# Optimization experiments

Hardware: AMD Instinct MI355X
Metric: run time of the kernel (lower is better)

## Reference

```python
import jax, jax.numpy as jnp
import numpy as np

HEADS = 8
DIM_HEAD = 64
SCALE = DIM_HEAD ** -0.5
POS_DIM = 64


def _sincos_pe(H, W, dim, dtype):
    # matches build_2d_sincos_pos_embed: [1, dim, H, W]
    y = jnp.linspace(-1.0, 1.0, H)[:, None] * jnp.ones((1, W), jnp.float32)
    x = jnp.ones((H, 1), jnp.float32) * jnp.linspace(-1.0, 1.0, W)[None, :]
    omega = 1.0 / (10000.0 ** (jnp.arange(dim // 4, dtype=jnp.float32) / (dim // 4)))
    px = x[..., None] * omega  # [H, W, dim//4]
    py = y[..., None] * omega
    pe = jnp.concatenate([jnp.sin(px), jnp.cos(px), jnp.sin(py), jnp.cos(py)], axis=-1)
    return pe.transpose(2, 0, 1)[None].astype(dtype)


def _conv2d(x, w):
    return jax.lax.conv_general_dilated(
        x, w, (1, 1), 'SAME', dimension_numbers=('NCHW', 'OIHW', 'NCHW'))


def _sobel(d):
    kx = jnp.array([[1, 0, -1], [2, 0, -2], [1, 0, -1]], jnp.float32).reshape(1, 1, 3, 3)
    ky = jnp.array([[1, 2, 1], [0, 0, 0], [-1, -2, -1]], jnp.float32).reshape(1, 1, 3, 3)
    return _conv2d(d, kx), _conv2d(d, ky)


def setup_inputs() -> dict:
    key = jax.random.key(0)
    ks = jax.random.split(key, 8)
    B, C, H, W = 2, 256, 64, 64
    hid = HEADS * DIM_HEAD  # 512
    s = 0.02
    return {
        'x': jax.random.normal(ks[0], (B, C, H, W), jnp.float32),
        'dsm': jax.random.uniform(ks[1], (B, 1, H, W), jnp.float32),
        'wq': jax.random.normal(ks[2], (hid, C), jnp.float32) * s,
        'wkv': jax.random.normal(ks[3], (2 * hid, C + 1), jnp.float32) * s,
        'wout': jax.random.normal(ks[4], (C, hid), jnp.float32) * s,
        'bout': jnp.zeros((C,), jnp.float32),
        'w_hape': jax.random.normal(ks[5], (hid, POS_DIM + 3), jnp.float32) * s,
        'b_hape': jnp.zeros((hid,), jnp.float32),
        'w_alpha': jax.random.normal(ks[6], (1, 1, 3, 3), jnp.float32) * 0.1,
        'b_alpha': jnp.zeros((1,), jnp.float32),
    }


def reference(x, dsm, wq, wkv, wout, bout, w_hape, b_hape, w_alpha, b_alpha):
    B, C, H, W = x.shape
    hid = wq.shape[0]
    # per-sample min-max normalize DSM over spatial dims
    dmin = dsm.min(axis=(2, 3), keepdims=True)
    dmax = dsm.max(axis=(2, 3), keepdims=True)
    d = (dsm - dmin) / (dmax - dmin + 1e-6)
    # HAPE: [PE | h | grad_h] -> 1x1 conv to hidden
    pe = jnp.broadcast_to(_sincos_pe(H, W, POS_DIM, x.dtype), (B, POS_DIM, H, W))
    gx, gy = _sobel(d)
    hape_in = jnp.concatenate([pe, d, gx, gy], axis=1)  # [B, 67, H, W]
    hape_k = jnp.einsum('oc,bchw->bohw', w_hape, hape_in) + b_hape[None, :, None, None]
    # QKV via 1x1 convs
    q = jnp.einsum('oc,bchw->bohw', wq, x)
    kv = jnp.einsum('oc,bchw->bohw', wkv, jnp.concatenate([x, d], axis=1))
    k = kv[:, :hid] + hape_k
    v = kv[:, hid:]
    to_heads = lambda t: t.reshape(B, HEADS, DIM_HEAD, H * W)  # b (h c) x y -> b h c (xy)
    qh = to_heads(q) * SCALE
    kh = to_heads(k)
    vh = to_heads(v)
    sim = jnp.einsum('bhdi,bhdj->bhij', qh, kh)  # [B, h, N, N]
    attn = jax.nn.softmax(sim, axis=-1)
    out = jnp.einsum('bhij,bhdj->bhid', attn, vh)  # [B, h, N, d]
    # b h (x y) d -> b (h d) x y
    out = out.transpose(0, 1, 3, 2).reshape(B, HEADS * DIM_HEAD, H, W)
    out = jnp.einsum('oc,bchw->bohw', wout, out) + bout[None, :, None, None]
    # fine: gradient-magnitude alpha gating
    mag = jnp.sqrt(jnp.maximum(gx, 0.0) ** 2 + jnp.maximum(gy, 0.0) ** 2 + 1e-12)
    alpha = jax.nn.sigmoid(_conv2d(mag, w_alpha) + b_alpha[None, :, None, None])
    return x + out * alpha
```

## Files before the change

kernel.cpp:

```cpp
#include <hip/hip_runtime.h>
#include <math.h>

#define NPOS 4096
#define MTOT 8192
#define KP   352
#define HT 64
#define WT 64
#define NSPLIT 2
#define KEYS_PER (NPOS / NSPLIT)
#define NCH (KEYS_PER / 64)

typedef unsigned short ushortT;
typedef short v8s __attribute__((ext_vector_type(8)));
typedef float v4f __attribute__((ext_vector_type(4)));
typedef unsigned uint2v __attribute__((ext_vector_type(2)));

static __device__ __forceinline__ ushortT bfr(float f) {
    union { float f; unsigned u; } v; v.f = f;
    return (ushortT)((v.u + 0x8000u) >> 16);
}
static __device__ __forceinline__ unsigned pack2bf(float a, float b) {
    union { float f; unsigned u; } ua, ub; ua.f = a; ub.f = b;
    return __builtin_amdgcn_perm(ub.u + 0x8000u, ua.u + 0x8000u, 0x07060302u);
}
static __device__ __forceinline__ unsigned pack2bf_t(float a, float b) {
    union { float f; unsigned u; } ua, ub; ua.f = a; ub.f = b;
    return __builtin_amdgcn_perm(ub.u, ua.u, 0x07060302u);
}
static __device__ __forceinline__ float fexp2(float x) {
#if __has_builtin(__builtin_amdgcn_exp2f)
    return __builtin_amdgcn_exp2f(x);
#else
    return exp2f(x);
#endif
}
static __device__ __forceinline__ void gll16(const ushortT* g, ushortT* l) {
    __builtin_amdgcn_global_load_lds((const __attribute__((address_space(1))) void*)g,
                                     (__attribute__((address_space(3))) void*)l, 16, 0, 0);
}

__global__ void k_prep(const float* __restrict__ dsm,
                       const float* __restrict__ walpha, const float* __restrict__ balpha,
                       ushortT* __restrict__ F, float* __restrict__ alpha) {
    int idx = blockIdx.x * 256 + threadIdx.x;
    int b = idx / NPOS, n = idx % NPOS;
    int hh = n / WT, ww = n % WT;
    const float* dp = dsm + (size_t)b * NPOS;

    float mn = 1e30f, mx = -1e30f;
    for (int i = threadIdx.x; i < NPOS; i += 256) {
        float v = dp[i];
        mn = fminf(mn, v); mx = fmaxf(mx, v);
    }
    for (int off = 32; off; off >>= 1) {
        mn = fminf(mn, __shfl_xor(mn, off, 64));
        mx = fmaxf(mx, __shfl_xor(mx, off, 64));
    }
    __shared__ float smn[4], smx[4];
    int wid = threadIdx.x >> 6;
    if ((threadIdx.x & 63) == 0) { smn[wid] = mn; smx[wid] = mx; }
    __syncthreads();
    float dmin = fminf(fminf(smn[0], smn[1]), fminf(smn[2], smn[3]));
    float dmax = fmaxf(fmaxf(smx[0], smx[1]), fmaxf(smx[2], smx[3]));
    float inv = 1.0f / (dmax - dmin + 1e-6f);

    float dwin[5][5];
    #pragma unroll
    for (int dy = 0; dy < 5; dy++)
        #pragma unroll
        for (int dx = 0; dx < 5; dx++) {
            int y = hh + dy - 2, x = ww + dx - 2;
            float v = 0.0f;
            if (y >= 0 && y < HT && x >= 0 && x < WT) v = (dp[y * WT + x] - dmin) * inv;
            dwin[dy][dx] = v;
        }

    float gxc = 0.f, gyc = 0.f;
    float conv = 0.f;
    #pragma unroll
    for (int oy = 0; oy < 3; oy++)
        #pragma unroll
        for (int ox = 0; ox < 3; ox++) {
            int qy = hh + oy - 1, qx = ww + ox - 1;
            float m = 0.0f;
            if (qy >= 0 && qy < HT && qx >= 0 && qx < WT) {
                float gx = dwin[oy][ox] - dwin[oy][ox + 2]
                         + 2.f * dwin[oy + 1][ox] - 2.f * dwin[oy + 1][ox + 2]
                         + dwin[oy + 2][ox] - dwin[oy + 2][ox + 2];
                float gy = dwin[oy][ox] + 2.f * dwin[oy][ox + 1] + dwin[oy][ox + 2]
                         - dwin[oy + 2][ox] - 2.f * dwin[oy + 2][ox + 1] - dwin[oy + 2][ox + 2];
                if (oy == 1 && ox == 1) { gxc = gx; gyc = gy; }
                float rx = fmaxf(gx, 0.f), ry = fmaxf(gy, 0.f);
                m = sqrtf(rx * rx + ry * ry + 1e-12f);
            }
            conv += walpha[oy * 3 + ox] * m;
        }
    alpha[idx] = 1.f / (1.f + __expf(-(conv + balpha[0])));

    ushortT* fb = F + (size_t)idx * KP;
    fb[256] = bfr(dwin[2][2]);
    fb[257] = bfr(gxc);
    fb[258] = bfr(gyc);
    float xc = -1.f + 2.f * (float)ww / 63.f;
    float yc = -1.f + 2.f * (float)hh / 63.f;
    const float l2w = 13.287712379549449f;
    #pragma unroll
    for (int i = 0; i < 16; i++) {
        float omega = exp2f(-(float)i * (l2w / 16.f));
        float px = xc * omega, py = yc * omega;
        fb[259 + i]      = bfr(__sinf(px));
        fb[259 + 16 + i] = bfr(__cosf(px));
        fb[259 + 32 + i] = bfr(__sinf(py));
        fb[259 + 48 + i] = bfr(__cosf(py));
    }
    #pragma unroll
    for (int z = 323; z < KP; z++) fb[z] = 0;
}

__global__ void k_cast(const float* __restrict__ x, ushortT* __restrict__ F) {
    __shared__ __align__(16) ushortT Tl[64][72];
    int nt = blockIdx.x * 64;
    int b = blockIdx.y >> 2, ct = (blockIdx.y & 3) * 64;
    int t = threadIdx.x;
    #pragma unroll
    for (int rep = 0; rep < 4; rep++) {
        int row = rep * 16 + (t >> 4), c4 = (t & 15) * 4;
        float4 f4 = *(const float4*)&x[((size_t)(b * 256 + ct + row)) * NPOS + nt + c4];
        Tl[c4 + 0][row] = bfr(f4.x);
        Tl[c4 + 1][row] = bfr(f4.y);
        Tl[c4 + 2][row] = bfr(f4.z);
        Tl[c4 + 3][row] = bfr(f4.w);
    }
    __syncthreads();
    #pragma unroll
    for (int rep = 0; rep < 2; rep++) {
        int slot = rep * 256 + t, row = slot >> 3, c8 = slot & 7;
        *(uint4*)&F[((size_t)(b * 4096 + nt + row)) * KP + ct + c8 * 8] = *(uint4*)&Tl[row][c8 * 8];
    }
}

__global__ void k_wcprep(const float* __restrict__ wq, const float* __restrict__ wkv,
                         const float* __restrict__ whape, const float* __restrict__ bhape,
                         const float* __restrict__ wout,
                         ushortT* __restrict__ Wc, float* __restrict__ biasc,
                         ushortT* __restrict__ woutb) {
    int idx = blockIdx.x * 256 + threadIdx.x;
    if (blockIdx.x < 512) {
        woutb[idx] = bfr(wout[idx]);
    }
    int o = idx / KP, k = idx % KP;
    float v = 0.f;
    if (o < 512) {
        if (k < 256) v = wq[o * 256 + k] * 0.18033688011112042f;
        if (k == 0) biasc[o] = 0.f;
    } else if (o < 1024) {
        int r = o - 512;
        if (k < 257) v = wkv[r * 257 + k];
        if (k == 256)      v += whape[r * 67 + 64];
        else if (k == 257) v = whape[r * 67 + 65];
        else if (k == 258) v = whape[r * 67 + 66];
        else if (k >= 259 && k < 323) v = whape[r * 67 + (k - 259)];
        if (k == 0) biasc[o] = bhape[r];
    } else {
        int r = o - 512;
        if (k < 257) v = wkv[r * 257 + k];
        if (k == 0) biasc[o] = 0.f;
    }
    Wc[idx] = bfr(v);
}

__global__ __launch_bounds__(256) void k_gemm1(const ushortT* __restrict__ Wc, const ushortT* __restrict__ F,
                                               const float* __restrict__ biasc,
                                               ushortT* __restrict__ qT, ushortT* __restrict__ kT,
                                               ushortT* __restrict__ vv) {
    __shared__ __align__(16) ushortT Al[64][40];
    __shared__ __align__(16) ushortT Bl[64][40];
    __shared__ __align__(16) ushortT Vt[64][72];
    int mt = blockIdx.x * 64;
    int ot = blockIdx.y * 64;
    int t = threadIdx.x, w = t >> 6, lane = t & 63, u = lane & 15, quad = lane >> 4;
    int arow = t >> 2, ac8 = t & 3;
    v4f acc[4] = {};
    for (int k0 = 0; k0 < KP; k0 += 32) {
        __syncthreads();
        *(uint4*)&Al[arow][ac8 * 8] = *(const uint4*)&Wc[(size_t)(ot + arow) * KP + k0 + ac8 * 8];
        *(uint4*)&Bl[arow][ac8 * 8] = *(const uint4*)&F[(size_t)(mt + arow) * KP + k0 + ac8 * 8];
        __syncthreads();
        v8s a = *(v8s*)&Al[w * 16 + u][quad * 8];
        #pragma unroll
        for (int n4 = 0; n4 < 4; n4++) {
            v8s bb = *(v8s*)&Bl[n4 * 16 + u][quad * 8];
            acc[n4] = __builtin_amdgcn_mfma_f32_16x16x32_bf16(a, bb, acc[n4], 0, 0, 0);
        }
    }
    int obase = ot + w * 16 + quad * 4;
    float bo[4];
    #pragma unroll
    for (int r = 0; r < 4; r++) bo[r] = biasc[obase + r];
    if (ot < 1024) {
        int h = (ot >> 6) & 7;
        ushortT* dst = (ot < 512) ? qT : kT;
        #pragma unroll
        for (int n4 = 0; n4 < 4; n4++) {
            int m = mt + n4 * 16 + u;
            uint2 val;
            val.x = pack2bf(acc[n4][0] + bo[0], acc[n4][1] + bo[1]);
            val.y = pack2bf(acc[n4][2] + bo[2], acc[n4][3] + bo[3]);
            *(uint2*)&dst[((size_t)h * MTOT + m) * 64 + w * 16 + quad * 4] = val;
        }
    } else {
        __syncthreads();
        #pragma unroll
        for (int n4 = 0; n4 < 4; n4++) {
            int ml = n4 * 16 + u;
            #pragma unroll
            for (int r = 0; r < 4; r++) Vt[w * 16 + quad * 4 + r][ml] = bfr(acc[n4][r] + bo[r]);
        }
        __syncthreads();
        #pragma unroll
        for (int rep = 0; rep < 2; rep++) {
            int slot = rep * 256 + t, row = slot >> 3, c8 = slot & 7;
            *(uint4*)&vv[(size_t)(ot - 1024 + row) * MTOT + mt + c8 * 8] = *(uint4*)&Vt[row][c8 * 8];
        }
    }
}

#define LIDX(row, cb) (((row) << 6) + ((((cb) ^ ((row) & 7))) << 3))
__global__ __launch_bounds__(256) void k_flash(const ushortT* __restrict__ qT,
                                               const ushortT* __restrict__ kT,
                                               const ushortT* __restrict__ vv,
                                               float* __restrict__ Opart,
                                               float* __restrict__ liPart) {
    __shared__ __align__(16) ushortT Kbuf[2][64 * 64];
    __shared__ __align__(16) ushortT Vbuf[2][64 * 64];

    int it = blockIdx.x;
    int bh = blockIdx.y;
    int half = blockIdx.z;
    int b = bh >> 3, h = bh & 7;
    int colbase = b * NPOS;
    int t = threadIdx.x, w = t >> 6, lane = t & 63, u = lane & 15, quad = lane >> 4;
    int qb = it * 128 + w * 32;

    const ushortT* Qg = qT + ((size_t)h * MTOT + colbase + qb) * 64;
    const ushortT* Kg = kT + ((size_t)h * MTOT + colbase + half * KEYS_PER) * 64;
    const ushortT* Vg = vv + ((size_t)(h * 64)) * MTOT + colbase + half * KEYS_PER;

    int r0 = t >> 3,         c0 = (t & 7) ^ (r0 & 7);
    int r1 = (256 + t) >> 3, c1 = (t & 7) ^ (r1 & 7);
    const ushortT* ks0 = Kg + r0 * 64 + c0 * 8;
    const ushortT* ks1 = Kg + r1 * 64 + c1 * 8;
    const ushortT* vs0 = Vg + (size_t)r0 * MTOT + c0 * 8;
    const ushortT* vs1 = Vg + (size_t)r1 * MTOT + c1 * 8;
    ushortT* kd0 = &Kbuf[0][0] + w * 512;
    ushortT* vd0 = &Vbuf[0][0] + w * 512;

    v8s bq[2][2];
    #pragma unroll
    for (int g = 0; g < 2; g++)
        #pragma unroll
        for (int hf = 0; hf < 2; hf++)
            bq[g][hf] = *(const v8s*)&Qg[(size_t)(g * 16 + u) * 64 + hf * 32 + quad * 8];

    v8s ones;
    #pragma unroll
    for (int i = 0; i < 8; i++) ones[i] = (short)0x3F80;

    v4f li4[2] = {};
    v4f O[4][2] = {};

    gll16(ks0, kd0);
    gll16(ks1, kd0 + 2048);
    gll16(vs0, vd0);
    gll16(vs1, vd0 + 2048);

    for (int jc = 0; jc < NCH; jc++) {
        int cur = jc & 1;
        __syncthreads();
        if (jc + 1 < NCH) {
            ushortT* kn = kd0 + (cur ^ 1) * 4096;
            ushortT* vn = vd0 + (cur ^ 1) * 4096;
            gll16(ks0 + 4096, kn);
            gll16(ks1 + 4096, kn + 2048);
            gll16(vs0 + 64,   vn);
            gll16(vs1 + 64,   vn + 2048);
            ks0 += 4096; ks1 += 4096; vs0 += 64; vs1 += 64;
        }

        const ushortT* Kb = &Kbuf[cur][0];
        const ushortT* Vb = &Vbuf[cur][0];

        v8s bp[2][2];
        #pragma unroll
        for (int kp = 0; kp < 2; kp++) {
            unsigned pk0[2][2], pk1[2][2];
            #pragma unroll
            for (int kk = 0; kk < 2; kk++) {
                int k4 = kp * 2 + kk;
                v8s ak0 = *(const v8s*)&Kb[LIDX(k4 * 16 + u, quad)];
                v8s ak1 = *(const v8s*)&Kb[LIDX(k4 * 16 + u, 4 + quad)];
                v4f st[2];
                #pragma unroll
                for (int g = 0; g < 2; g++) {
                    st[g] = (v4f){0.f, 0.f, 0.f, 0.f};
                    st[g] = __builtin_amdgcn_mfma_f32_16x16x32_bf16(ak0, bq[g][0], st[g], 0, 0, 0);
                    st[g] = __builtin_amdgcn_mfma_f32_16x16x32_bf16(ak1, bq[g][1], st[g], 0, 0, 0);
                }
                #pragma unroll
                for (int g = 0; g < 2; g++) {
                    float p0 = fexp2(st[g][0]);
                    float p1 = fexp2(st[g][1]);
                    float p2 = fexp2(st[g][2]);
                    float p3 = fexp2(st[g][3]);
                    pk0[g][kk] = pack2bf_t(p0, p1);
                    pk1[g][kk] = pack2bf_t(p2, p3);
                }
            }
            #pragma unroll
            for (int g = 0; g < 2; g++) {
                uint2v r0s = __builtin_amdgcn_permlane32_swap(pk0[g][0], pk0[g][1], false, false);
                uint2v r1s = __builtin_amdgcn_permlane32_swap(pk1[g][0], pk1[g][1], false, false);
                uint2v t0 = __builtin_amdgcn_permlane16_swap(r0s.x, r0s.y, false, false);
                uint2v t1 = __builtin_amdgcn_permlane16_swap(r1s.x, r1s.y, false, false);
                union { uint4 u4; v8s s; } cv;
                cv.u4.x = t0.x; cv.u4.y = t1.x; cv.u4.z = t0.y; cv.u4.w = t1.y;
                bp[g][kp] = cv.s;
            }
        }

        #pragma unroll
        for (int g = 0; g < 2; g++) {
            li4[g] = __builtin_amdgcn_mfma_f32_16x16x32_bf16(ones, bp[g][0], li4[g], 0, 0, 0);
            li4[g] = __builtin_amdgcn_mfma_f32_16x16x32_bf16(ones, bp[g][1], li4[g], 0, 0, 0);
        }

        #pragma unroll
        for (int d4 = 0; d4 < 4; d4++) {
            v8s av0 = *(const v8s*)&Vb[LIDX(d4 * 16 + u, quad)];
            v8s av1 = *(const v8s*)&Vb[LIDX(d4 * 16 + u, 4 + quad)];
            #pragma unroll
            for (int g = 0; g < 2; g++) {
                O[d4][g] = __builtin_amdgcn_mfma_f32_16x16x32_bf16(av0, bp[g][0], O[d4][g], 0, 0, 0);
                O[d4][g] = __builtin_amdgcn_mfma_f32_16x16x32_bf16(av1, bp[g][1], O[d4][g], 0, 0, 0);
            }
        }
    }

    #pragma unroll
    for (int g = 0; g < 2; g++) {
        int q = qb + g * 16 + u;
        size_t m2 = (size_t)(half * 2 + b) * 4096 + q;
        size_t base = m2 * 512 + h * 64;
        #pragma unroll
        for (int d4 = 0; d4 < 4; d4++) {
            float4 o4;
            o4.x = O[d4][g][0]; o4.y = O[d4][g][1]; o4.z = O[d4][g][2]; o4.w = O[d4][g][3];
            *(float4*)&Opart[base + d4 * 16 + quad * 4] = o4;
        }
        if (quad == 0) liPart[m2 * 8 + h] = li4[g][0];
    }
}

__global__ __launch_bounds__(256) void k_comb(const float* __restrict__ Opart,
                                              const float* __restrict__ liPart,
                                              ushortT* __restrict__ aoB) {
    int tid = blockIdx.x * 256 + threadIdx.x;
    int m = tid >> 7, c4 = (tid & 127) * 4, h = c4 >> 6;
    float l = 0.f;
    #pragma unroll
    for (int s = 0; s < NSPLIT; s++) l += liPart[((size_t)s * 8192 + m) * 8 + h];
    float inv = 1.f / l;
    float ox = 0.f, oy = 0.f, oz = 0.f, ow = 0.f;
    #pragma unroll
    for (int s = 0; s < NSPLIT; s++) {
        float4 o = *(const float4*)&Opart[((size_t)s * 8192 + m) * 512 + c4];
        ox += o.x; oy += o.y; oz += o.z; ow += o.w;
    }
    uint2 val;
    val.x = pack2bf(ox * inv, oy * inv);
    val.y = pack2bf(oz * inv, ow * inv);
    *(uint2*)&aoB[(size_t)m * 512 + c4] = val;
}

__global__ __launch_bounds__(256) void k_gemm2(const ushortT* __restrict__ woutb, const ushortT* __restrict__ aoB,
                                               const float* __restrict__ bout, const float* __restrict__ x,
                                               const float* __restrict__ alpha, float* __restrict__ out) {
    __shared__ __align__(16) ushortT Al[64][40];
    __shared__ __align__(16) ushortT Bl[64][40];
    int mt = blockIdx.x * 64;
    int ot = blockIdx.y * 64;
    int t = threadIdx.x, w = t >> 6, lane = t & 63, u = lane & 15, quad = lane >> 4;
    int arow = t >> 2, ac8 = t & 3;
    v4f acc[4] = {};
    for (int k0 = 0; k0 < 512; k0 += 32) {
        __syncthreads();
        *(uint4*)&Al[arow][ac8 * 8] = *(const uint4*)&woutb[(size_t)(ot + arow) * 512 + k0 + ac8 * 8];
        *(uint4*)&Bl[arow][ac8 * 8] = *(const uint4*)&aoB[(size_t)(mt + arow) * 512 + k0 + ac8 * 8];
        __syncthreads();
        v8s a = *(v8s*)&Al[w * 16 + u][quad * 8];
        #pragma unroll
        for (int n4 = 0; n4 < 4; n4++) {
            v8s bb = *(v8s*)&Bl[n4 * 16 + u][quad * 8];
            acc[n4] = __builtin_amdgcn_mfma_f32_16x16x32_bf16(a, bb, acc[n4], 0, 0, 0);
        }
    }
    int b = mt >> 12, n0 = mt & 4095;
    int obase = ot + w * 16 + quad * 4;
    float bo[4];
    #pragma unroll
    for (int r = 0; r < 4; r++) bo[r] = bout[obase + r];
    #pragma unroll
    for (int n4 = 0; n4 < 4; n4++) {
        int n = n0 + n4 * 16 + u;
        float al = alpha[(size_t)b * NPOS + n];
        #pragma unroll
        for (int r = 0; r < 4; r++) {
            size_t xi = ((size_t)(b * 256 + obase + r)) * NPOS + n;
            out[xi] = x[xi] + (acc[n4][r] + bo[r]) * al;
        }
    }
}

extern "C" void kernel_launch(void* const* d_in, const int* in_sizes, int n_in,
                              void* d_out, int out_size, void* d_ws, size_t ws_size,
                              hipStream_t stream) {
    const float* x      = (const float*)d_in[0];
    const float* dsm    = (const float*)d_in[1];
    const float* wq     = (const float*)d_in[2];
    const float* wkv    = (const float*)d_in[3];
    const float* wout   = (const float*)d_in[4];
    const float* bout   = (const float*)d_in[5];
    const float* whape  = (const float*)d_in[6];
    const float* bhape  = (const float*)d_in[7];
    const float* walpha = (const float*)d_in[8];
    const float* balpha = (const float*)d_in[9];
    float* out = (float*)d_out;
    float* ws  = (float*)d_ws;

    size_t off = 0;
    float* alpha = ws + off; off += (size_t)2 * NPOS;
    float* biasc = ws + off; off += 2048;
    float* Opart  = ws + off; off += (size_t)NSPLIT * MTOT * 512;
    float* liPart = ws + off; off += (size_t)NSPLIT * MTOT * 8;
    ushortT* F     = (ushortT*)(ws + off); off += (size_t)MTOT * KP / 2;
    ushortT* Wc    = (ushortT*)(ws + off); off += (size_t)1536 * KP / 2;
    ushortT* woutb = (ushortT*)(ws + off); off += (size_t)256 * 512 / 2;
    ushortT* qT    = (ushortT*)(ws + off); off += (size_t)8 * MTOT * 64 / 2;
    ushortT* kT    = (ushortT*)(ws + off); off += (size_t)8 * MTOT * 64 / 2;
    ushortT* vv    = (ushortT*)(ws + off); off += (size_t)512 * MTOT / 2;
    ushortT* aoB   = (ushortT*)(ws + off); off += (size_t)MTOT * 512 / 2;
    (void)in_sizes; (void)n_in; (void)out_size; (void)ws_size;

    k_prep<<<32, 256, 0, stream>>>(dsm, walpha, balpha, F, alpha);
    k_cast<<<dim3(64, 8), 256, 0, stream>>>(x, F);
    k_wcprep<<<(1536 * KP) / 256, 256, 0, stream>>>(wq, wkv, whape, bhape, wout, Wc, biasc, woutb);
    k_gemm1<<<dim3(128, 24), 256, 0, stream>>>(Wc, F, biasc, qT, kT, vv);
    k_flash<<<dim3(32, 16, NSPLIT), 256, 0, stream>>>(qT, kT, vv, Opart, liPart);
    k_comb<<<4096, 256, 0, stream>>>(Opart, liPart, aoB);
    k_gemm2<<<dim3(128, 4), 256, 0, stream>>>(woutb, aoB, bout, x, alpha, out);
}
```

Baseline: 214.2 us.

## Enlarge QKV GEMM tile and replace async LDS loads with register-staged prefetch

```diff
diff --git a/kernel.cpp b/kernel.cpp
--- a/kernel.cpp
+++ b/kernel.cpp
@@ -33,10 +33,6 @@
 #else
     return exp2f(x);
 #endif
-}
-static __device__ __forceinline__ void gll16(const ushortT* g, ushortT* l) {
-    __builtin_amdgcn_global_load_lds((const __attribute__((address_space(1))) void*)g,
-                                     (__attribute__((address_space(3))) void*)l, 16, 0, 0);
 }
 
 __global__ void k_prep(const float* __restrict__ dsm,
@@ -173,52 +169,66 @@
                                                const float* __restrict__ biasc,
                                                ushortT* __restrict__ qT, ushortT* __restrict__ kT,
                                                ushortT* __restrict__ vv) {
-    __shared__ __align__(16) ushortT Al[64][40];
+    __shared__ __align__(16) ushortT Al[128][40];
     __shared__ __align__(16) ushortT Bl[64][40];
-    __shared__ __align__(16) ushortT Vt[64][72];
+    __shared__ __align__(16) ushortT Vt[128][72];
     int mt = blockIdx.x * 64;
-    int ot = blockIdx.y * 64;
+    int ot = blockIdx.y * 128;
     int t = threadIdx.x, w = t >> 6, lane = t & 63, u = lane & 15, quad = lane >> 4;
-    int arow = t >> 2, ac8 = t & 3;
-    v4f acc[4] = {};
+    int ar0 = t >> 2, ac0 = t & 3;
+    int ar1 = 64 + ar0;
+    int br = t >> 2, bc = t & 3;
+    v4f acc[2][4] = {};
     for (int k0 = 0; k0 < KP; k0 += 32) {
         __syncthreads();
-        *(uint4*)&Al[arow][ac8 * 8] = *(const uint4*)&Wc[(size_t)(ot + arow) * KP + k0 + ac8 * 8];
-        *(uint4*)&Bl[arow][ac8 * 8] = *(const uint4*)&F[(size_t)(mt + arow) * KP + k0 + ac8 * 8];
-        __syncthreads();
-        v8s a = *(v8s*)&Al[w * 16 + u][quad * 8];
+        *(uint4*)&Al[ar0][ac0 * 8] = *(const uint4*)&Wc[(size_t)(ot + ar0) * KP + k0 + ac0 * 8];
+        *(uint4*)&Al[ar1][ac0 * 8] = *(const uint4*)&Wc[(size_t)(ot + ar1) * KP + k0 + ac0 * 8];
+        *(uint4*)&Bl[br][bc * 8]   = *(const uint4*)&F[(size_t)(mt + br) * KP + k0 + bc * 8];
+        __syncthreads();
+        v8s a0 = *(v8s*)&Al[w * 32 + u][quad * 8];
+        v8s a1 = *(v8s*)&Al[w * 32 + 16 + u][quad * 8];
         #pragma unroll
         for (int n4 = 0; n4 < 4; n4++) {
             v8s bb = *(v8s*)&Bl[n4 * 16 + u][quad * 8];
-            acc[n4] = __builtin_amdgcn_mfma_f32_16x16x32_bf16(a, bb, acc[n4], 0, 0, 0);
-        }
-    }
-    int obase = ot + w * 16 + quad * 4;
-    float bo[4];
-    #pragma unroll
-    for (int r = 0; r < 4; r++) bo[r] = biasc[obase + r];
+            acc[0][n4] = __builtin_amdgcn_mfma_f32_16x16x32_bf16(a0, bb, acc[0][n4], 0, 0, 0);
+            acc[1][n4] = __builtin_amdgcn_mfma_f32_16x16x32_bf16(a1, bb, acc[1][n4], 0, 0, 0);
+        }
+    }
+    float bo[2][4];
+    #pragma unroll
+    for (int rr = 0; rr < 2; rr++)
+        #pragma unroll
+        for (int r = 0; r < 4; r++) bo[rr][r] = biasc[ot + w * 32 + rr * 16 + quad * 4 + r];
     if (ot < 1024) {
-        int h = (ot >> 6) & 7;
         ushortT* dst = (ot < 512) ? qT : kT;
         #pragma unroll
-        for (int n4 = 0; n4 < 4; n4++) {
-            int m = mt + n4 * 16 + u;
-            uint2 val;
-            val.x = pack2bf(acc[n4][0] + bo[0], acc[n4][1] + bo[1]);
-            val.y = pack2bf(acc[n4][2] + bo[2], acc[n4][3] + bo[3]);
-            *(uint2*)&dst[((size_t)h * MTOT + m) * 64 + w * 16 + quad * 4] = val;
+        for (int rr = 0; rr < 2; rr++) {
+            int oo = ot + w * 32 + rr * 16;
+            int h = (oo >> 6) & 7;
+            int dcol = (oo & 63) + quad * 4;
+            #pragma unroll
+            for (int n4 = 0; n4 < 4; n4++) {
+                int m = mt + n4 * 16 + u;
+                uint2 val;
+                val.x = pack2bf(acc[rr][n4][0] + bo[rr][0], acc[rr][n4][1] + bo[rr][1]);
+                val.y = pack2bf(acc[rr][n4][2] + bo[rr][2], acc[rr][n4][3] + bo[rr][3]);
+                *(uint2*)&dst[((size_t)h * MTOT + m) * 64 + dcol] = val;
+            }
         }
     } else {
         __syncthreads();
         #pragma unroll
-        for (int n4 = 0; n4 < 4; n4++) {
-            int ml = n4 * 16 + u;
+        for (int rr = 0; rr < 2; rr++)
             #pragma unroll
-            for (int r = 0; r < 4; r++) Vt[w * 16 + quad * 4 + r][ml] = bfr(acc[n4][r] + bo[r]);
-        }
-        __syncthreads();
-        #pragma unroll
-        for (int rep = 0; rep < 2; rep++) {
+            for (int n4 = 0; n4 < 4; n4++) {
+                int ml = n4 * 16 + u;
+                #pragma unroll
+                for (int r = 0; r < 4; r++)
+                    Vt[w * 32 + rr * 16 + quad * 4 + r][ml] = bfr(acc[rr][n4][r] + bo[rr][r]);
+            }
+        __syncthreads();
+        #pragma unroll
+        for (int rep = 0; rep < 4; rep++) {
             int slot = rep * 256 + t, row = slot >> 3, c8 = slot & 7;
             *(uint4*)&vv[(size_t)(ot - 1024 + row) * MTOT + mt + c8 * 8] = *(uint4*)&Vt[row][c8 * 8];
         }
@@ -226,11 +236,11 @@
 }
 
 #define LIDX(row, cb) (((row) << 6) + ((((cb) ^ ((row) & 7))) << 3))
-__global__ __launch_bounds__(256) void k_flash(const ushortT* __restrict__ qT,
-                                               const ushortT* __restrict__ kT,
-                                               const ushortT* __restrict__ vv,
-                                               float* __restrict__ Opart,
-                                               float* __restrict__ liPart) {
+__global__ __launch_bounds__(256, 4) void k_flash(const ushortT* __restrict__ qT,
+                                                  const ushortT* __restrict__ kT,
+                                                  const ushortT* __restrict__ vv,
+                                                  float* __restrict__ Opart,
+                                                  float* __restrict__ liPart) {
     __shared__ __align__(16) ushortT Kbuf[2][64 * 64];
     __shared__ __align__(16) ushortT Vbuf[2][64 * 64];
 
@@ -246,14 +256,8 @@
     const ushortT* Kg = kT + ((size_t)h * MTOT + colbase + half * KEYS_PER) * 64;
     const ushortT* Vg = vv + ((size_t)(h * 64)) * MTOT + colbase + half * KEYS_PER;
 
-    int r0 = t >> 3,         c0 = (t & 7) ^ (r0 & 7);
-    int r1 = (256 + t) >> 3, c1 = (t & 7) ^ (r1 & 7);
-    const ushortT* ks0 = Kg + r0 * 64 + c0 * 8;
-    const ushortT* ks1 = Kg + r1 * 64 + c1 * 8;
-    const ushortT* vs0 = Vg + (size_t)r0 * MTOT + c0 * 8;
-    const ushortT* vs1 = Vg + (size_t)r1 * MTOT + c1 * 8;
-    ushortT* kd0 = &Kbuf[0][0] + w * 512;
-    ushortT* vd0 = &Vbuf[0][0] + w * 512;
+    int row0 = t >> 3, c80 = t & 7;
+    int row1 = 32 + row0;
 
     v8s bq[2][2];
     #pragma unroll
@@ -269,22 +273,25 @@
     v4f li4[2] = {};
     v4f O[4][2] = {};
 
-    gll16(ks0, kd0);
-    gll16(ks1, kd0 + 2048);
-    gll16(vs0, vd0);
-    gll16(vs1, vd0 + 2048);
-
+    uint4 kr0 = *(const uint4*)&Kg[(size_t)row0 * 64 + c80 * 8];
+    uint4 kr1 = *(const uint4*)&Kg[(size_t)row1 * 64 + c80 * 8];
+    uint4 vr0 = *(const uint4*)&Vg[(size_t)row0 * MTOT + c80 * 8];
+    uint4 vr1 = *(const uint4*)&Vg[(size_t)row1 * MTOT + c80 * 8];
+
+    #pragma unroll 2
     for (int jc = 0; jc < NCH; jc++) {
         int cur = jc & 1;
+        *(uint4*)&Kbuf[cur][LIDX(row0, c80)] = kr0;
+        *(uint4*)&Kbuf[cur][LIDX(row1, c80)] = kr1;
+        *(uint4*)&Vbuf[cur][LIDX(row0, c80)] = vr0;
+        *(uint4*)&Vbuf[cur][LIDX(row1, c80)] = vr1;
         __syncthreads();
         if (jc + 1 < NCH) {
-            ushortT* kn = kd0 + (cur ^ 1) * 4096;
-            ushortT* vn = vd0 + (cur ^ 1) * 4096;
-            gll16(ks0 + 4096, kn);
-            gll16(ks1 + 4096, kn + 2048);
-            gll16(vs0 + 64,   vn);
-            gll16(vs1 + 64,   vn + 2048);
-            ks0 += 4096; ks1 += 4096; vs0 += 64; vs1 += 64;
+            int jb = (jc + 1) * 64;
+            kr0 = *(const uint4*)&Kg[(size_t)(jb + row0) * 64 + c80 * 8];
+            kr1 = *(const uint4*)&Kg[(size_t)(jb + row1) * 64 + c80 * 8];
+            vr0 = *(const uint4*)&Vg[(size_t)row0 * MTOT + jb + c80 * 8];
+            vr1 = *(const uint4*)&Vg[(size_t)row1 * MTOT + jb + c80 * 8];
         }
 
         const ushortT* Kb = &Kbuf[cur][0];
@@ -454,7 +461,7 @@
     k_prep<<<32, 256, 0, stream>>>(dsm, walpha, balpha, F, alpha);
     k_cast<<<dim3(64, 8), 256, 0, stream>>>(x, F);
     k_wcprep<<<(1536 * KP) / 256, 256, 0, stream>>>(wq, wkv, whape, bhape, wout, Wc, biasc, woutb);
-    k_gemm1<<<dim3(128, 24), 256, 0, stream>>>(Wc, F, biasc, qT, kT, vv);
+    k_gemm1<<<dim3(128, 12), 256, 0, stream>>>(Wc, F, biasc, qT, kT, vv);
     k_flash<<<dim3(32, 16, NSPLIT), 256, 0, stream>>>(qT, kT, vv, Opart, liPart);
     k_comb<<<4096, 256, 0, stream>>>(Opart, liPart, aoB);
     k_gemm2<<<dim3(128, 4), 256, 0, stream>>>(woutb, aoB, bout, x, alpha, out);
```

Measured after the change: 202.6 us. -5.4%, faster.
